# Kernel tuning notes

Measured on AMD Instinct MI355X. Metric: run time of the kernel, lower is better.

Reference implementation:

```python
import math
import jax, jax.numpy as jnp
import numpy as np

CHANNELS = 256
NUM_HEADS = 4
GROUPS = 32
EPS = 1e-5


def setup_inputs() -> dict:
    key = jax.random.key(0)
    ks = jax.random.split(key, 7)
    b, c, h, w = 8, CHANNELS, 48, 48
    return {
        "x": jax.random.normal(ks[0], (b, c, h, w), dtype=jnp.float32),
        "gn_w": jax.random.uniform(ks[1], (c,), dtype=jnp.float32),
        "gn_b": jax.random.normal(ks[2], (c,), dtype=jnp.float32) * 0.02,
        "qkv_w": jax.random.normal(ks[3], (3 * c, c), dtype=jnp.float32) * (1.0 / math.sqrt(c)),
        "qkv_b": jax.random.normal(ks[4], (3 * c,), dtype=jnp.float32) * 0.02,
        "proj_w": jax.random.normal(ks[5], (c, c), dtype=jnp.float32) * (1.0 / math.sqrt(c)),
        "proj_b": jax.random.normal(ks[6], (c,), dtype=jnp.float32) * 0.02,
    }


def reference(x, gn_w, gn_b, qkv_w, qkv_b, proj_w, proj_b):
    b, c, h, w = x.shape
    nh = NUM_HEADS
    hd = c // nh
    hw = h * w

    # GroupNorm(32, c): normalize over (c/G, h, w) per group
    xg = x.reshape(b, GROUPS, c // GROUPS, h, w)
    mean = jnp.mean(xg, axis=(2, 3, 4), keepdims=True)
    var = jnp.mean(jnp.square(xg - mean), axis=(2, 3, 4), keepdims=True)
    xn = (xg - mean) * jax.lax.rsqrt(var + EPS)
    xn = xn.reshape(b, c, h, w) * gn_w[None, :, None, None] + gn_b[None, :, None, None]

    # 1x1 conv qkv: per-pixel linear
    qkv = jnp.einsum('bchw,oc->bohw', xn, qkv_w) + qkv_b[None, :, None, None]
    q, k, v = jnp.split(qkv, 3, axis=1)  # each (b, c, h, w)

    # split channels into heads: (b, nh, hd, hw)
    q = q.reshape(b, nh, hd, hw)
    k = k.reshape(b, nh, hd, hw)
    v = v.reshape(b, nh, hd, hw)

    scale = 1.0 / math.sqrt(hd)
    attn = jnp.einsum('bndi,bndj->bnij', q, k) * scale  # (b, nh, hw, hw)
    attn = jax.nn.softmax(attn, axis=-1)
    out = jnp.einsum('bnij,bndj->bndi', attn, v)  # (b, nh, hd, hw)
    out = out.reshape(b, c, h, w)

    out = jnp.einsum('bchw,oc->bohw', out, proj_w) + proj_b[None, :, None, None]
    return x + out
```

## Files before the change

### kernel.cpp

```cpp
#include <hip/hip_runtime.h>
#include <hip/hip_bf16.h>
#include <math.h>

#define NB 8
#define NC 256
#define NHW 2304
#define NH 4
#define HD 64
#define CPG 8
#define GN_EPS 1e-5f

typedef __bf16 bf16;
typedef __bf16 bf16x4 __attribute__((ext_vector_type(4)));
typedef __bf16 bf16x8 __attribute__((ext_vector_type(8)));
typedef float f32x4 __attribute__((ext_vector_type(4)));
typedef float f32x16 __attribute__((ext_vector_type(16)));
typedef int i32x4 __attribute__((ext_vector_type(4)));
typedef unsigned int u32;

#define MFMA16(a, b, c) __builtin_amdgcn_mfma_f32_16x16x32_bf16(a, b, c, 0, 0, 0)
#define MFMA32(a, b, c) __builtin_amdgcn_mfma_f32_32x32x16_bf16(a, b, c, 0, 0, 0)

__device__ __forceinline__ float fexp2(float x) {
  float r;
  asm("v_exp_f32 %0, %1" : "=v"(r) : "v"(x));
  return r;
}

__global__ __launch_bounds__(256) void k_pre(const float* __restrict__ x,
                                             const float* __restrict__ gw,
                                             const float* __restrict__ gb,
                                             const float* __restrict__ qw,
                                             const float* __restrict__ pw,
                                             bf16* __restrict__ xnt,
                                             bf16* __restrict__ wq,
                                             bf16* __restrict__ wp) {
  int t = threadIdx.x;
  if (blockIdx.x < 768) {
    int i = blockIdx.x * 256 + t;
    wq[i] = (bf16)qw[i];
    if (i < NC * NC) wp[i] = (bf16)pw[i];
    return;
  }
  int bid = blockIdx.x - 768;
  int b = bid >> 5;
  int g = bid & 31;
  int c0 = g * CPG;
  const float* xb = x + (b * NC + c0) * NHW;
  float v[CPG][9];
  float s = 0.f, s2 = 0.f;
#pragma unroll
  for (int cc = 0; cc < CPG; ++cc)
#pragma unroll
    for (int k = 0; k < 9; ++k) {
      float val = xb[cc * NHW + k * 256 + t];
      v[cc][k] = val;
      s += val;
      s2 += val * val;
    }
#pragma unroll
  for (int m = 1; m < 64; m <<= 1) {
    s += __shfl_xor(s, m);
    s2 += __shfl_xor(s2, m);
  }
  __shared__ float red[8];
  int wid = t >> 6;
  if ((t & 63) == 0) { red[wid] = s; red[4 + wid] = s2; }
  __syncthreads();
  s = red[0] + red[1] + red[2] + red[3];
  s2 = red[4] + red[5] + red[6] + red[7];
  const float inv_n = 1.0f / (CPG * NHW);
  float mean = s * inv_n;
  float var = s2 * inv_n - mean * mean;
  float rsq = rsqrtf(var + GN_EPS);
  float ka[CPG], kb[CPG];
#pragma unroll
  for (int cc = 0; cc < CPG; ++cc) {
    float wv = gw[c0 + cc];
    ka[cc] = wv * rsq;
    kb[cc] = gb[c0 + cc] - mean * rsq * wv;
  }
  bf16* dst = xnt + b * NHW * NC + c0;
#pragma unroll
  for (int k = 0; k < 9; ++k) {
    bf16x8 o;
#pragma unroll
    for (int cc = 0; cc < CPG; ++cc)
      o[cc] = (bf16)(v[cc][k] * ka[cc] + kb[cc]);
    *reinterpret_cast<bf16x8*>(dst + (k * 256 + t) * NC) = o;
  }
}

__global__ __launch_bounds__(256) void k_qkv(const bf16* __restrict__ xnt,
                                             const bf16* __restrict__ wq,
                                             const float* __restrict__ qkvb,
                                             bf16* __restrict__ qt,
                                             bf16* __restrict__ kt,
                                             bf16* __restrict__ vv) {
  int b = blockIdx.z;
  int i_base = blockIdx.x * 128;
  int o_base = blockIdx.y * 128;
  int t = threadIdx.x;
  int lane = t & 63, wid = t >> 6;
  int wm = (wid >> 1) * 64, wn = (wid & 1) * 64;
  int l15 = lane & 15, g = lane >> 4;
  const bool qk = (o_base < 512);
  const bf16* ab;
  const bf16* bb;
  if (qk) {
    ab = wq + (o_base + wm + l15) * NC + g * 8;
    bb = xnt + ((size_t)b * NHW + i_base + wn + l15) * NC + g * 8;
  } else {
    ab = xnt + ((size_t)b * NHW + i_base + wm + l15) * NC + g * 8;
    bb = wq + (o_base + wn + l15) * NC + g * 8;
  }
  f32x4 acc[4][4] = {};
#pragma unroll 2
  for (int kc = 0; kc < 8; ++kc) {
    bf16x8 af[4], bf[4];
#pragma unroll
    for (int mf = 0; mf < 4; ++mf)
      af[mf] = *reinterpret_cast<const bf16x8*>(ab + mf * 16 * NC + kc * 32);
#pragma unroll
    for (int nf = 0; nf < 4; ++nf)
      bf[nf] = *reinterpret_cast<const bf16x8*>(bb + nf * 16 * NC + kc * 32);
#pragma unroll
    for (int mf = 0; mf < 4; ++mf)
#pragma unroll
      for (int nf = 0; nf < 4; ++nf)
        acc[mf][nf] = MFMA16(af[mf], bf[nf], acc[mf][nf]);
  }
  if (qk) {
    const float qscale = 0.125f * 1.4426950408889634f;
#pragma unroll
    for (int mf = 0; mf < 4; ++mf) {
      int o0 = o_base + wm + mf * 16 + g * 4;
      f32x4 b4 = *reinterpret_cast<const f32x4*>(qkvb + o0);
      bool isQ = (o0 < 256);
      float sc = isQ ? qscale : 1.0f;
      int oo = isQ ? o0 : o0 - 256;
      bf16* base = (isQ ? qt : kt) +
                   ((size_t)(b * NH + (oo >> 6)) * NHW) * HD + (oo & 63);
#pragma unroll
      for (int nf = 0; nf < 4; ++nf) {
        int i = i_base + wn + nf * 16 + l15;
        bf16x4 w;
#pragma unroll
        for (int r = 0; r < 4; ++r)
          w[r] = (bf16)((acc[mf][nf][r] + b4[r]) * sc);
        *reinterpret_cast<bf16x4*>(base + (size_t)i * HD) = w;
      }
    }
  } else {
#pragma unroll
    for (int nf = 0; nf < 4; ++nf) {
      int og = o_base + wn + nf * 16 + l15;
      float bias = qkvb[og];
      int o2 = og - 512;
      bf16* dp = vv + ((size_t)(b * NH + (o2 >> 6)) * HD + (o2 & 63)) * NHW +
                 i_base + wm + g * 4;
#pragma unroll
      for (int mf = 0; mf < 4; ++mf) {
        bf16x4 w;
#pragma unroll
        for (int r = 0; r < 4; ++r) w[r] = (bf16)(acc[mf][nf][r] + bias);
        *reinterpret_cast<bf16x4*>(dp + mf * 16) = w;
      }
    }
  }
}

__global__ __launch_bounds__(512, 4) void k_attn(const bf16* __restrict__ qt,
                                                 const bf16* __restrict__ kt,
                                                 const bf16* __restrict__ vv,
                                                 bf16* __restrict__ att) {
  __shared__ union SM {
    struct { bf16 k[2][4096]; bf16 v[2][4096]; } kv;
    float m[4][64][17];
  } smem;

  const int tid = threadIdx.x;
  const int wid = tid >> 6, lane = tid & 63;
  const int l31 = lane & 31, g2 = lane >> 5;
  const int ig = wid & 3, jsub = wid >> 2;

  const int bid = blockIdx.x;
  const int wg = (bid & 7) * 72 + (bid >> 3);
  const int bh = wg / 18, it = wg % 18;
  const int b = bh >> 2, n = bh & 3;
  const int i0w = it * 128 + ig * 32;

  const bf16* qb = qt + (size_t)bh * NHW * HD;
  const bf16* kb = kt + (size_t)bh * NHW * HD;
  const bf16* vb = vv + (size_t)bh * HD * NHW;

  const int r0 = tid >> 3, cs = tid & 7;
  const bf16* kg = kb + r0 * HD + cs * 8;
  const bf16* vg = vb + (size_t)r0 * NHW + cs * 8;
#define EOFF(c, row) ((c) * 512 + ((((row) + (c)) & 63) << 3))
  const int lw = EOFF(cs, r0);

  int ksw[4];
#pragma unroll
  for (int kk = 0; kk < 4; ++kk) ksw[kk] = EOFF(2 * kk + g2, jsub * 32 + l31);
  int vsw0[2], vsw1[2];
#pragma unroll
  for (int J = 0; J < 2; ++J) {
    int c = jsub * 4 + J * 2 + g2;
    vsw0[J] = EOFF(c, l31);
    vsw1[J] = EOFF(c, l31 + 32);
  }
#undef EOFF

  bf16x8 q[4];
#pragma unroll
  for (int kk = 0; kk < 4; ++kk)
    q[kk] = *reinterpret_cast<const bf16x8*>(qb + (i0w + l31) * HD + kk * 16 + g2 * 8);

  f32x16 acc0 = {}, acc1 = {};
  float l_r = 0.f;

  {
    bf16x8 a = *reinterpret_cast<const bf16x8*>(kg);
    bf16x8 d = *reinterpret_cast<const bf16x8*>(vg);
    *reinterpret_cast<bf16x8*>(&smem.kv.k[0][lw]) = a;
    *reinterpret_cast<bf16x8*>(&smem.kv.v[0][lw]) = d;
  }
  asm volatile("s_waitcnt lgkmcnt(0)" ::: "memory");
  __builtin_amdgcn_s_barrier();

  for (int t = 0; t < 36; ++t) {
    const int cur = t & 1;
    bf16x8 kr, vr;
    if (t < 35) {
      kr = *reinterpret_cast<const bf16x8*>(kg + (t + 1) * (64 * HD));
      vr = *reinterpret_cast<const bf16x8*>(vg + (t + 1) * 64);
    }
    const bf16* kc = smem.kv.k[cur];
    const bf16* vc = smem.kv.v[cur];

    f32x16 s = {};
    __builtin_amdgcn_s_setprio(1);
#pragma unroll
    for (int kk = 0; kk < 4; ++kk) {
      bf16x8 kf = *reinterpret_cast<const bf16x8*>(kc + ksw[kk]);
      s = MFMA32(kf, q[kk], s);
    }
    __builtin_amdgcn_s_setprio(0);

    u32 P[8];
    float la = 0.f, lb = 0.f;
#pragma unroll
    for (int m = 0; m < 8; ++m) {
      float e0 = fexp2(s[2 * m]);
      float e1 = fexp2(s[2 * m + 1]);
      la += e0;
      lb += e1;
      u32 pk;
      asm("v_cvt_pk_bf16_f32 %0, %1, %2" : "=v"(pk) : "v"(e0), "v"(e1));
      P[m] = pk;
    }
    l_r += la + lb;

#pragma unroll
    for (int J = 0; J < 2; ++J) {
      u32 w0 = P[4 * J], w2 = P[4 * J + 2];
      asm("v_permlane32_swap_b32 %0, %1" : "+v"(w0), "+v"(w2));
      u32 w1 = P[4 * J + 1], w3 = P[4 * J + 3];
      asm("v_permlane32_swap_b32 %0, %1" : "+v"(w1), "+v"(w3));
      i32x4 wv;
      wv[0] = (int)w0; wv[1] = (int)w1; wv[2] = (int)w2; wv[3] = (int)w3;
      bf16x8 pf = __builtin_bit_cast(bf16x8, wv);
      bf16x8 v0 = *reinterpret_cast<const bf16x8*>(vc + vsw0[J]);
      bf16x8 v1 = *reinterpret_cast<const bf16x8*>(vc + vsw1[J]);
      __builtin_amdgcn_s_setprio(1);
      acc0 = MFMA32(v0, pf, acc0);
      acc1 = MFMA32(v1, pf, acc1);
      __builtin_amdgcn_s_setprio(0);
    }

    if (t < 35) {
      const int nb = cur ^ 1;
      *reinterpret_cast<bf16x8*>(&smem.kv.k[nb][lw]) = kr;
      *reinterpret_cast<bf16x8*>(&smem.kv.v[nb][lw]) = vr;
    }
    asm volatile("s_waitcnt lgkmcnt(0)" ::: "memory");
    __builtin_amdgcn_s_barrier();
  }

  if (jsub == 1) {
    float* mb = smem.m[ig][lane];
#pragma unroll
    for (int e = 0; e < 16; ++e) mb[e] = acc0[e];
    mb[16] = l_r;
  }
  __syncthreads();
  if (jsub == 0) {
    const float* mb = smem.m[ig][lane];
#pragma unroll
    for (int e = 0; e < 16; ++e) acc0[e] += mb[e];
    l_r += mb[16];
  }
  __syncthreads();
  if (jsub == 1) {
    float* mb = smem.m[ig][lane];
#pragma unroll
    for (int e = 0; e < 16; ++e) mb[e] = acc1[e];
  }
  __syncthreads();
  if (jsub == 0) {
    const float* mb = smem.m[ig][lane];
#pragma unroll
    for (int e = 0; e < 16; ++e) acc1[e] += mb[e];
    l_r += __shfl_xor(l_r, 32);
    const float inv = 1.0f / l_r;
    bf16* ob = att + ((size_t)(b * NHW) + i0w + l31) * NC + n * HD;
#pragma unroll
    for (int rq = 0; rq < 4; ++rq) {
      bf16x4 o0, o1;
#pragma unroll
      for (int c = 0; c < 4; ++c) {
        o0[c] = (bf16)(acc0[rq * 4 + c] * inv);
        o1[c] = (bf16)(acc1[rq * 4 + c] * inv);
      }
      *reinterpret_cast<bf16x4*>(ob + 8 * rq + 4 * g2) = o0;
      *reinterpret_cast<bf16x4*>(ob + 32 + 8 * rq + 4 * g2) = o1;
    }
  }
}

__global__ __launch_bounds__(256) void k_proj(const bf16* __restrict__ att,
                                              const bf16* __restrict__ wp,
                                              const float* __restrict__ pb,
                                              const float* __restrict__ x,
                                              float* __restrict__ out) {
  int b = blockIdx.z;
  int i_base = blockIdx.x * 128;
  int o_base = blockIdx.y * 128;
  int t = threadIdx.x;
  int lane = t & 63, wid = t >> 6;
  int wm = (wid >> 1) * 64, wn = (wid & 1) * 64;
  int l15 = lane & 15, g = lane >> 4;
  const bf16* ab = wp + (o_base + wm + l15) * NC + g * 8;
  const bf16* bb = att + (b * NHW + i_base + wn + l15) * NC + g * 8;
  f32x4 acc[4][4] = {};
#pragma unroll 2
  for (int kc = 0; kc < 8; ++kc) {
    bf16x8 af[4], bf[4];
#pragma unroll
    for (int mf = 0; mf < 4; ++mf)
      af[mf] = *reinterpret_cast<const bf16x8*>(ab + mf * 16 * NC + kc * 32);
#pragma unroll
    for (int nf = 0; nf < 4; ++nf)
      bf[nf] = *reinterpret_cast<const bf16x8*>(bb + nf * 16 * NC + kc * 32);
#pragma unroll
    for (int mf = 0; mf < 4; ++mf)
#pragma unroll
      for (int nf = 0; nf < 4; ++nf)
        acc[mf][nf] = MFMA16(af[mf], bf[nf], acc[mf][nf]);
  }
  int orow0 = o_base + wm + g * 4;
#pragma unroll
  for (int mf = 0; mf < 4; ++mf)
#pragma unroll
    for (int r = 0; r < 4; ++r) {
      int o = orow0 + mf * 16 + r;
      float bias = pb[o];
      const float* xr = x + (b * NC + o) * NHW + i_base + wn;
      float* orow = out + (b * NC + o) * NHW + i_base + wn;
#pragma unroll
      for (int nf = 0; nf < 4; ++nf) {
        int i = nf * 16 + l15;
        orow[i] = acc[mf][nf][r] + bias + xr[i];
      }
    }
}

extern "C" void kernel_launch(void* const* d_in, const int* in_sizes, int n_in,
                              void* d_out, int out_size, void* d_ws, size_t ws_size,
                              hipStream_t stream) {
  const float* x    = (const float*)d_in[0];
  const float* gnw  = (const float*)d_in[1];
  const float* gnb  = (const float*)d_in[2];
  const float* qkvw = (const float*)d_in[3];
  const float* qkvb = (const float*)d_in[4];
  const float* pw   = (const float*)d_in[5];
  const float* pb   = (const float*)d_in[6];
  float* out = (float*)d_out;

  bf16* ws = (bf16*)d_ws;
  const size_t NE = (size_t)NB * NHW * NC;
  bf16* xnt = ws;
  bf16* qt  = ws + NE;
  bf16* kt  = ws + 2 * NE;
  bf16* vv  = ws + 3 * NE;
  bf16* att = ws + 4 * NE;
  bf16* wqb = ws + 5 * NE;
  bf16* wpb = wqb + 768 * 256;

  k_pre<<<1024, 256, 0, stream>>>(x, gnw, gnb, qkvw, pw, xnt, wqb, wpb);
  k_qkv<<<dim3(18, 6, NB), 256, 0, stream>>>(xnt, wqb, qkvb, qt, kt, vv);
  k_attn<<<576, 512, 0, stream>>>(qt, kt, vv, att);
  k_proj<<<dim3(18, 2, NB), 256, 0, stream>>>(att, wpb, pb, x, out);
}
```

Measured before the change: 143.8 us.

## Load K fragments directly from global into registers, stage only V in LDS

The attention kernel stops staging K tiles through shared memory. Each lane now loads its own K MFMA fragments straight from global memory into a register double buffer (kA/kB), and the loop is unrolled by two so the buffers alternate. This removes the LDS writes and reads for K and halves shared-memory use. In exchange it uses more registers, which is why launch bounds drop to 3 waves per SIMD, and each K element is fetched from global or L2 by several waves instead of once per block.

After: 218.2 us. +51.8%, slower.

```diff
diff --git a/kernel.cpp b/kernel.cpp
--- a/kernel.cpp
+++ b/kernel.cpp
@@ -170,12 +170,12 @@
   }
 }
 
-__global__ __launch_bounds__(512, 4) void k_attn(const bf16* __restrict__ qt,
+__global__ __launch_bounds__(512, 3) void k_attn(const bf16* __restrict__ qt,
                                                  const bf16* __restrict__ kt,
                                                  const bf16* __restrict__ vv,
                                                  bf16* __restrict__ att) {
   __shared__ union SM {
-    struct { bf16 k[2][4096]; bf16 v[2][4096]; } kv;
+    bf16 v[2][4096];
     float m[4][64][17];
   } smem;
 
@@ -195,14 +195,9 @@
   const bf16* vb = vv + (size_t)bh * HD * NHW;
 
   const int r0 = tid >> 3, cs = tid & 7;
-  const bf16* kg = kb + r0 * HD + cs * 8;
   const bf16* vg = vb + (size_t)r0 * NHW + cs * 8;
 #define EOFF(c, row) ((c) * 512 + ((((row) + (c)) & 63) << 3))
   const int lw = EOFF(cs, r0);
-
-  int ksw[4];
-#pragma unroll
-  for (int kk = 0; kk < 4; ++kk) ksw[kk] = EOFF(2 * kk + g2, jsub * 32 + l31);
   int vsw0[2], vsw1[2];
 #pragma unroll
   for (int J = 0; J < 2; ++J) {
@@ -212,6 +207,8 @@
   }
 #undef EOFF
 
+  const bf16* kfb = kb + (size_t)(jsub * 32 + l31) * HD + g2 * 8;
+
   bf16x8 q[4];
 #pragma unroll
   for (int kk = 0; kk < 4; ++kk)
@@ -219,74 +216,86 @@
 
   f32x16 acc0 = {}, acc1 = {};
   float l_r = 0.f;
+  bf16x8 kA[4], kB[4];
 
   {
-    bf16x8 a = *reinterpret_cast<const bf16x8*>(kg);
     bf16x8 d = *reinterpret_cast<const bf16x8*>(vg);
-    *reinterpret_cast<bf16x8*>(&smem.kv.k[0][lw]) = a;
-    *reinterpret_cast<bf16x8*>(&smem.kv.v[0][lw]) = d;
-  }
+    *reinterpret_cast<bf16x8*>(&smem.v[0][lw]) = d;
+  }
+#pragma unroll
+  for (int kk = 0; kk < 4; ++kk)
+    kA[kk] = *reinterpret_cast<const bf16x8*>(kfb + kk * 16);
   asm volatile("s_waitcnt lgkmcnt(0)" ::: "memory");
   __builtin_amdgcn_s_barrier();
 
-  for (int t = 0; t < 36; ++t) {
-    const int cur = t & 1;
-    bf16x8 kr, vr;
-    if (t < 35) {
-      kr = *reinterpret_cast<const bf16x8*>(kg + (t + 1) * (64 * HD));
-      vr = *reinterpret_cast<const bf16x8*>(vg + (t + 1) * 64);
-    }
-    const bf16* kc = smem.kv.k[cur];
-    const bf16* vc = smem.kv.v[cur];
-
-    f32x16 s = {};
-    __builtin_amdgcn_s_setprio(1);
-#pragma unroll
-    for (int kk = 0; kk < 4; ++kk) {
-      bf16x8 kf = *reinterpret_cast<const bf16x8*>(kc + ksw[kk]);
-      s = MFMA32(kf, q[kk], s);
-    }
-    __builtin_amdgcn_s_setprio(0);
-
-    u32 P[8];
-    float la = 0.f, lb = 0.f;
-#pragma unroll
-    for (int m = 0; m < 8; ++m) {
-      float e0 = fexp2(s[2 * m]);
-      float e1 = fexp2(s[2 * m + 1]);
-      la += e0;
-      lb += e1;
-      u32 pk;
-      asm("v_cvt_pk_bf16_f32 %0, %1, %2" : "=v"(pk) : "v"(e0), "v"(e1));
-      P[m] = pk;
-    }
-    l_r += la + lb;
-
-#pragma unroll
-    for (int J = 0; J < 2; ++J) {
-      u32 w0 = P[4 * J], w2 = P[4 * J + 2];
-      asm("v_permlane32_swap_b32 %0, %1" : "+v"(w0), "+v"(w2));
-      u32 w1 = P[4 * J + 1], w3 = P[4 * J + 3];
-      asm("v_permlane32_swap_b32 %0, %1" : "+v"(w1), "+v"(w3));
-      i32x4 wv;
-      wv[0] = (int)w0; wv[1] = (int)w1; wv[2] = (int)w2; wv[3] = (int)w3;
-      bf16x8 pf = __builtin_bit_cast(bf16x8, wv);
-      bf16x8 v0 = *reinterpret_cast<const bf16x8*>(vc + vsw0[J]);
-      bf16x8 v1 = *reinterpret_cast<const bf16x8*>(vc + vsw1[J]);
-      __builtin_amdgcn_s_setprio(1);
-      acc0 = MFMA32(v0, pf, acc0);
-      acc1 = MFMA32(v1, pf, acc1);
-      __builtin_amdgcn_s_setprio(0);
-    }
-
-    if (t < 35) {
-      const int nb = cur ^ 1;
-      *reinterpret_cast<bf16x8*>(&smem.kv.k[nb][lw]) = kr;
-      *reinterpret_cast<bf16x8*>(&smem.kv.v[nb][lw]) = vr;
-    }
+#define TILE_BODY(KF, VBUF)                                                   \
+  {                                                                           \
+    const bf16* vc = smem.v[VBUF];                                            \
+    bf16x8 vf0[2], vf1[2];                                                    \
+    _Pragma("unroll") for (int J = 0; J < 2; ++J) {                           \
+      vf0[J] = *reinterpret_cast<const bf16x8*>(vc + vsw0[J]);                \
+      vf1[J] = *reinterpret_cast<const bf16x8*>(vc + vsw1[J]);                \
+    }                                                                         \
+    f32x16 s = {};                                                            \
+    __builtin_amdgcn_s_setprio(1);                                            \
+    _Pragma("unroll") for (int kk = 0; kk < 4; ++kk) s =                      \
+        MFMA32(KF[kk], q[kk], s);                                             \
+    __builtin_amdgcn_s_setprio(0);                                            \
+    u32 P[8];                                                                 \
+    float la = 0.f, lb = 0.f;                                                 \
+    _Pragma("unroll") for (int m = 0; m < 8; ++m) {                           \
+      float e0 = fexp2(s[2 * m]);                                             \
+      float e1 = fexp2(s[2 * m + 1]);                                         \
+      la += e0;                                                               \
+      lb += e1;                                                               \
+      u32 pk;                                                                 \
+      asm("v_cvt_pk_bf16_f32 %0, %1, %2" : "=v"(pk) : "v"(e0), "v"(e1));      \
+      P[m] = pk;                                                              \
+    }                                                                         \
+    l_r += la + lb;                                                           \
+    _Pragma("unroll") for (int J = 0; J < 2; ++J) {                           \
+      u32 w0 = P[4 * J], w2 = P[4 * J + 2];                                   \
+      asm("v_permlane32_swap_b32 %0, %1" : "+v"(w0), "+v"(w2));               \
+      u32 w1 = P[4 * J + 1], w3 = P[4 * J + 3];                               \
+      asm("v_permlane32_swap_b32 %0, %1" : "+v"(w1), "+v"(w3));               \
+      i32x4 wv;                                                               \
+      wv[0] = (int)w0; wv[1] = (int)w1; wv[2] = (int)w2; wv[3] = (int)w3;     \
+      bf16x8 pf = __builtin_bit_cast(bf16x8, wv);                             \
+      __builtin_amdgcn_s_setprio(1);                                          \
+      acc0 = MFMA32(vf0[J], pf, acc0);                                        \
+      acc1 = MFMA32(vf1[J], pf, acc1);                                        \
+      __builtin_amdgcn_s_setprio(0);                                          \
+    }                                                                         \
+  }
+
+  for (int tt = 0; tt < 36; tt += 2) {
+    bf16x8 vr = *reinterpret_cast<const bf16x8*>(vg + (tt + 1) * 64);
+#pragma unroll
+    for (int kk = 0; kk < 4; ++kk)
+      kB[kk] = *reinterpret_cast<const bf16x8*>(
+          kfb + (size_t)((tt + 1) * 64) * HD + kk * 16);
+    __builtin_amdgcn_sched_barrier(0);
+    TILE_BODY(kA, 0)
+    *reinterpret_cast<bf16x8*>(&smem.v[1][lw]) = vr;
     asm volatile("s_waitcnt lgkmcnt(0)" ::: "memory");
     __builtin_amdgcn_s_barrier();
-  }
+
+    bf16x8 vr2;
+    const bool more = (tt + 2 < 36);
+    if (more) {
+      vr2 = *reinterpret_cast<const bf16x8*>(vg + (tt + 2) * 64);
+#pragma unroll
+      for (int kk = 0; kk < 4; ++kk)
+        kA[kk] = *reinterpret_cast<const bf16x8*>(
+            kfb + (size_t)((tt + 2) * 64) * HD + kk * 16);
+    }
+    __builtin_amdgcn_sched_barrier(0);
+    TILE_BODY(kB, 1)
+    if (more) *reinterpret_cast<bf16x8*>(&smem.v[0][lw]) = vr2;
+    asm volatile("s_waitcnt lgkmcnt(0)" ::: "memory");
+    __builtin_amdgcn_s_barrier();
+  }
+#undef TILE_BODY
 
   if (jsub == 1) {
     float* mb = smem.m[ig][lane];
```
